# Performance work log

Hardware: AMD Instinct MI355X
Metric: run time of the kernel (lower is better)

Reference implementation:

```python
import jax, jax.numpy as jnp
import numpy as np

B, N, C = 16, 64, 512


def _ln(x, g, b, eps=1e-5):
    m = x.mean(-1, keepdims=True)
    v = ((x - m) ** 2).mean(-1, keepdims=True)
    return (x - m) * jax.lax.rsqrt(v + eps) * g + b


def _layer(x, edge, WA, WB, WE, WU, WV, ge, be, gv, bv):
    # x: (B, N, C); edge: (B, N, N, C) with edge[b, i, j] for pair (end=i, start=j)
    n = x.shape[1]
    res = x
    Vix = x @ WA.T  # end-node (i) features
    Vjx = x @ WB.T  # start-node (j) features
    e_lin = edge @ WE.T
    # 'ev,bvc->bec' with end/start one-hots == broadcast gather over i / j
    m = Vix[:, :, None, :] + Vjx[:, None, :, :] + e_lin
    edge = edge + jax.nn.relu(_ln(m, ge, be))
    e = jax.nn.softmax(jax.nn.sigmoid(edge), axis=2)  # softmax over start-node axis j
    Ujx = x @ WV.T  # gathered at start node j
    # end.T scatter == sum over j of e[b,i,j,c] * Ujx[b,j,c]
    agg = jnp.einsum('bijc,bjc->bic', e, Ujx) / n
    x = x @ WU.T + agg
    x = jax.nn.relu(res + _ln(x, gv, bv))
    return x, edge


def setup_inputs() -> dict:
    key = jax.random.key(0)
    ks = jax.random.split(key, 12)
    scale = float(np.sqrt(2.0 / C))
    inp = {
        "x": jax.random.normal(ks[0], (B, N, C), jnp.float32),
        "edge": jax.random.normal(ks[1], (B, N * N, C), jnp.float32),
    }
    names = ["WA1", "WB1", "WE1", "WU1", "WV1", "WA2", "WB2", "WE2", "WU2", "WV2"]
    for i, nm in enumerate(names):
        inp[nm] = jax.random.normal(ks[2 + i], (C, C), jnp.float32) * scale
    for nm in ["ge1", "gv1", "ge2", "gv2"]:
        inp[nm] = jnp.ones((C,), jnp.float32)
    for nm in ["be1", "bv1", "be2", "bv2"]:
        inp[nm] = jnp.zeros((C,), jnp.float32)
    return inp


def reference(x, edge, WA1, WB1, WE1, WU1, WV1, WA2, WB2, WE2, WU2, WV2,
              ge1, be1, gv1, bv1, ge2, be2, gv2, bv2):
    b, _, c = edge.shape
    n = x.shape[1]
    edge = edge.reshape(b, n, n, c)
    x, edge = _layer(x, edge, WA1, WB1, WE1, WU1, WV1, ge1, be1, gv1, bv1)
    x, edge = _layer(x, edge, WA2, WB2, WE2, WU2, WV2, ge2, be2, gv2, bv2)
    return x, edge.reshape(b, n * n, c)
```

## Files before the change

kernel.cpp:

```cpp
#include <hip/hip_runtime.h>
#include <math.h>

#define CD 512
#define NNODE 64
#define TPAD 520

typedef __attribute__((ext_vector_type(8)))  short bfrag8;
typedef __attribute__((ext_vector_type(8)))  short sv8;
typedef __attribute__((ext_vector_type(4)))  short sv4;
typedef __attribute__((ext_vector_type(16))) float f32x16;

__device__ __forceinline__ unsigned short f2bf(float f) {
    union { float f; unsigned u; } v; v.f = f;
    unsigned r = (v.u + 0x7fffu + ((v.u >> 16) & 1u)) >> 16;
    return (unsigned short)r;
}
__device__ __forceinline__ float bf2f(unsigned short u) {
    union { unsigned u; float f; } v; v.u = ((unsigned)u) << 16;
    return v.f;
}

__global__ void pack32_k(const float* __restrict__ W0, const float* __restrict__ W1,
                         const float* __restrict__ W2, const float* __restrict__ W3,
                         const float* __restrict__ W4, const float* __restrict__ W5,
                         const float* __restrict__ W6, const float* __restrict__ W7,
                         const float* __restrict__ W8, const float* __restrict__ W9,
                         unsigned short* __restrict__ out)
{
    const float* Ws[10] = {W0,W1,W2,W3,W4,W5,W6,W7,W8,W9};
    int kt = blockIdx.x, ct = blockIdx.y, wi = blockIdx.z, l = threadIdx.x;
    const float* W = Ws[wi];
    int c  = ct * 32 + (l & 31);
    int k0 = kt * 16 + (l >> 5) * 8;
    const float* src = W + (size_t)c * CD + k0;
    unsigned short o[8];
    #pragma unroll
    for (int i = 0; i < 8; ++i) o[i] = f2bf(src[i]);
    unsigned short* dst = out + (size_t)wi * 262144 + ((size_t)(kt * 16 + ct) * 64 + l) * 8;
    *(bfrag8*)dst = *(bfrag8*)o;
}

__global__ __launch_bounds__(512, 4) void proj_mfma(
    const float* __restrict__ A, const unsigned short* __restrict__ Bp4,
    float* __restrict__ O0, float* __restrict__ O1,
    float* __restrict__ O2, float* __restrict__ O3)
{
    __shared__ unsigned short tile[64 * TPAD];
    const int rb = blockIdx.x * 64, widx = blockIdx.y;
    float* outs[4] = {O0,O1,O2,O3};
    float* out = outs[widx];
    const unsigned short* Bp = Bp4 + (size_t)widx * 262144;
    const int t = threadIdx.x, l = t & 63, w = t >> 6;
    const int stripe = w & 1, H = w >> 1;

    const float* src = A + (size_t)rb * CD;
    #pragma unroll 4
    for (int it = 0; it < 16; ++it) {
        int flat = it * 2048 + t * 4;
        float4 v4 = *(const float4*)(src + flat);
        int r = flat >> 9, c = flat & 511;
        sv4 pk; pk.x = (short)f2bf(v4.x); pk.y = (short)f2bf(v4.y);
        pk.z = (short)f2bf(v4.z); pk.w = (short)f2bf(v4.w);
        *(sv4*)(tile + r * TPAD + c) = pk;
    }
    __syncthreads();

    f32x16 acc[4] = {};
    const unsigned short* aptr = tile + (size_t)(stripe * 32 + (l & 31)) * TPAD + (l >> 5) * 8;
    const unsigned short* bptr = Bp + ((size_t)(H * 4) * 64 + l) * 8;

    bfrag8 a0, a1, b0[4], b1[4];
    a0 = *(const bfrag8*)aptr;
    #pragma unroll
    for (int tt = 0; tt < 4; ++tt) b0[tt] = *(const bfrag8*)(bptr + tt * 512);
    for (int k2 = 0; k2 < 16; ++k2) {
        int kt1 = 2 * k2 + 1;
        a1 = *(const bfrag8*)(aptr + kt1 * 16);
        #pragma unroll
        for (int tt = 0; tt < 4; ++tt) b1[tt] = *(const bfrag8*)(bptr + (size_t)kt1 * 8192 + tt * 512);
        #pragma unroll
        for (int tt = 0; tt < 4; ++tt)
            acc[tt] = __builtin_amdgcn_mfma_f32_32x32x16_bf16(a0, b0[tt], acc[tt], 0, 0, 0);
        int kt2 = (k2 == 15) ? 31 : (2 * k2 + 2);
        a0 = *(const bfrag8*)(aptr + kt2 * 16);
        #pragma unroll
        for (int tt = 0; tt < 4; ++tt) b0[tt] = *(const bfrag8*)(bptr + (size_t)kt2 * 8192 + tt * 512);
        #pragma unroll
        for (int tt = 0; tt < 4; ++tt)
            acc[tt] = __builtin_amdgcn_mfma_f32_32x32x16_bf16(a1, b1[tt], acc[tt], 0, 0, 0);
    }
    const int cbase = H * 128 + (l & 31);
    #pragma unroll
    for (int r = 0; r < 16; ++r) {
        int rl = (r & 3) + 8 * (r >> 2) + 4 * (l >> 5);
        int row = rb + stripe * 32 + rl;
        #pragma unroll
        for (int tt = 0; tt < 4; ++tt)
            out[(size_t)row * CD + cbase + tt * 32] = acc[tt][r];
    }
}

template<bool INBF, bool OUTBF>
__global__ __launch_bounds__(512, 4) void edge_mfma(
    const void* __restrict__ einv, void* __restrict__ eoutv,
    const float* __restrict__ Vix, const float* __restrict__ Vjx,
    const float* __restrict__ Ujx, const unsigned short* __restrict__ Bp,
    const float* __restrict__ ge, const float* __restrict__ be,
    float* __restrict__ agg)
{
    __shared__ unsigned short tile[64 * TPAD];
    __shared__ float sums[64][4][2];

    const int bi = blockIdx.x;
    const int brow = bi & ~63;
    const int t = threadIdx.x, l = t & 63, w = t >> 6;
    const int stripe = w & 1, H = w >> 1;

    if (INBF) {
        const unsigned short* src = (const unsigned short*)einv + (size_t)bi * 65536;
        #pragma unroll 4
        for (int it = 0; it < 8; ++it) {
            int flat = it * 4096 + t * 8;
            int r = flat >> 9, c = flat & 511;
            *(sv8*)(tile + r * TPAD + c) = *(const sv8*)(src + flat);
        }
    } else {
        const float* src = (const float*)einv + (size_t)bi * 32768;
        #pragma unroll 4
        for (int it = 0; it < 16; ++it) {
            int flat = it * 2048 + t * 4;
            float4 v4 = *(const float4*)(src + flat);
            int r = flat >> 9, c = flat & 511;
            sv4 pk; pk.x = (short)f2bf(v4.x); pk.y = (short)f2bf(v4.y);
            pk.z = (short)f2bf(v4.z); pk.w = (short)f2bf(v4.w);
            *(sv4*)(tile + r * TPAD + c) = pk;
        }
    }
    __syncthreads();

    f32x16 acc[4] = {};
    const unsigned short* aptr = tile + (size_t)(stripe * 32 + (l & 31)) * TPAD + (l >> 5) * 8;
    const unsigned short* bptr = Bp + ((size_t)(H * 4) * 64 + l) * 8;

    bfrag8 a0, a1, b0[4], b1[4];
    a0 = *(const bfrag8*)aptr;
    #pragma unroll
    for (int tt = 0; tt < 4; ++tt) b0[tt] = *(const bfrag8*)(bptr + tt * 512);
    for (int k2 = 0; k2 < 16; ++k2) {
        int kt1 = 2 * k2 + 1;
        a1 = *(const bfrag8*)(aptr + kt1 * 16);
        #pragma unroll
        for (int tt = 0; tt < 4; ++tt) b1[tt] = *(const bfrag8*)(bptr + (size_t)kt1 * 8192 + tt * 512);
        #pragma unroll
        for (int tt = 0; tt < 4; ++tt)
            acc[tt] = __builtin_amdgcn_mfma_f32_32x32x16_bf16(a0, b0[tt], acc[tt], 0, 0, 0);
        int kt2 = (k2 == 15) ? 31 : (2 * k2 + 2);
        a0 = *(const bfrag8*)(aptr + kt2 * 16);
        #pragma unroll
        for (int tt = 0; tt < 4; ++tt) b0[tt] = *(const bfrag8*)(bptr + (size_t)kt2 * 8192 + tt * 512);
        #pragma unroll
        for (int tt = 0; tt < 4; ++tt)
            acc[tt] = __builtin_amdgcn_mfma_f32_32x32x16_bf16(a1, b1[tt], acc[tt], 0, 0, 0);
    }

    const int cbase = H * 128 + (l & 31);
    float vix[4], gev[4], bev[4];
    #pragma unroll
    for (int tt = 0; tt < 4; ++tt) {
        int c = cbase + tt * 32;
        vix[tt] = Vix[(size_t)bi * CD + c];
        gev[tt] = ge[c]; bev[tt] = be[c];
    }
    float s1[16], s2[16];
    #pragma unroll
    for (int r = 0; r < 16; ++r) {
        int rl = (r & 3) + 8 * (r >> 2) + 4 * (l >> 5);
        int rt = stripe * 32 + rl;
        const float* vjr = Vjx + (size_t)(brow + rt) * CD;
        float a1_ = 0.f, a2_ = 0.f;
        #pragma unroll
        for (int tt = 0; tt < 4; ++tt) {
            float m = acc[tt][r] + vix[tt] + vjr[cbase + tt * 32];
            acc[tt][r] = m;
            a1_ += m; a2_ = fmaf(m, m, a2_);
        }
        s1[r] = a1_; s2[r] = a2_;
    }
    #pragma unroll
    for (int off = 1; off < 32; off <<= 1) {
        #pragma unroll
        for (int r = 0; r < 16; ++r) {
            s1[r] += __shfl_xor(s1[r], off, 64);
            s2[r] += __shfl_xor(s2[r], off, 64);
        }
    }
    if ((l & 31) == 0) {
        #pragma unroll
        for (int r = 0; r < 16; ++r) {
            int rl = (r & 3) + 8 * (r >> 2) + 4 * (l >> 5);
            int rt = stripe * 32 + rl;
            sums[rt][H][0] = s1[r]; sums[rt][H][1] = s2[r];
        }
    }
    __syncthreads();

    #pragma unroll
    for (int r = 0; r < 16; ++r) {
        int rl = (r & 3) + 8 * (r >> 2) + 4 * (l >> 5);
        int rt = stripe * 32 + rl;
        float t1 = sums[rt][0][0] + sums[rt][1][0] + sums[rt][2][0] + sums[rt][3][0];
        float t2 = sums[rt][0][1] + sums[rt][1][1] + sums[rt][2][1] + sums[rt][3][1];
        float mean = t1 * (1.f / 512.f);
        float var  = t2 * (1.f / 512.f) - mean * mean;
        float rs   = rsqrtf(var + 1e-5f);
        unsigned short* trow = tile + (size_t)rt * TPAD;
        #pragma unroll
        for (int tt = 0; tt < 4; ++tt) {
            int c = cbase + tt * 32;
            float ln  = (acc[tt][r] - mean) * rs * gev[tt] + bev[tt];
            float env = bf2f(trow[c]) + fmaxf(ln, 0.f);
            if (OUTBF) ((unsigned short*)eoutv)[(size_t)bi * 65536 + rt * 512 + c] = f2bf(env);
            else       ((float*)eoutv)[(size_t)bi * 32768 + rt * 512 + c] = env;
            float sg = 1.f / (1.f + __expf(-env));
            trow[c] = f2bf(__expf(sg));
        }
    }
    __syncthreads();

    {
        int c = t;
        const float* uj = Ujx + (size_t)brow * CD + c;
        float den = 0.f, num = 0.f;
        #pragma unroll 8
        for (int j = 0; j < NNODE; ++j) {
            float wv = bf2f(tile[j * TPAD + c]);
            float uv = uj[(size_t)j * CD];
            den += wv; num = fmaf(wv, uv, num);
        }
        agg[(size_t)bi * CD + c] = num / (den * (float)NNODE);
    }
}

__global__ __launch_bounds__(256) void xupd_kernel(
    const float* __restrict__ res,
    const float* __restrict__ XU,
    const float* __restrict__ aggp,
    const float* __restrict__ gv, const float* __restrict__ bv,
    float* __restrict__ xout)
{
    int r = blockIdx.x * 4 + (threadIdx.x >> 6);
    int lane = threadIdx.x & 63;
    const float* xu = XU + (size_t)r * CD;
    const float* ag = aggp + (size_t)r * CD;
    float y[8]; float s1 = 0.f, s2 = 0.f;
    #pragma unroll
    for (int u = 0; u < 8; ++u) {
        int c = lane + u * 64;
        float v = xu[c] + ag[c];
        y[u] = v; s1 += v; s2 += v * v;
    }
    #pragma unroll
    for (int off = 32; off > 0; off >>= 1) {
        s1 += __shfl_xor(s1, off, 64);
        s2 += __shfl_xor(s2, off, 64);
    }
    float mean = s1 * (1.f / 512.f);
    float var  = s2 * (1.f / 512.f) - mean * mean;
    float rs   = rsqrtf(var + 1e-5f);
    const float* rr = res + (size_t)r * CD;
    float* xo = xout + (size_t)r * CD;
    #pragma unroll
    for (int u = 0; u < 8; ++u) {
        int c = lane + u * 64;
        float ln = (y[u] - mean) * rs * gv[c] + bv[c];
        xo[c] = fmaxf(rr[c] + ln, 0.f);
    }
}

extern "C" void kernel_launch(void* const* d_in, const int* in_sizes, int n_in,
                              void* d_out, int out_size, void* d_ws, size_t ws_size,
                              hipStream_t stream)
{
    const float* x    = (const float*)d_in[0];
    const float* edge = (const float*)d_in[1];
    const float* W[10];
    for (int i = 0; i < 10; ++i) W[i] = (const float*)d_in[2 + i];
    const float* ge1 = (const float*)d_in[12];
    const float* gv1 = (const float*)d_in[13];
    const float* ge2 = (const float*)d_in[14];
    const float* gv2 = (const float*)d_in[15];
    const float* be1 = (const float*)d_in[16];
    const float* bv1 = (const float*)d_in[17];
    const float* be2 = (const float*)d_in[18];
    const float* bv2 = (const float*)d_in[19];

    char* wsb = (char*)d_ws;
    unsigned short* P32 = (unsigned short*)wsb;
    float* Vix = (float*)(wsb + (size_t)6  * 1048576);
    float* Vjx = (float*)(wsb + (size_t)8  * 1048576);
    float* Ujx = (float*)(wsb + (size_t)10 * 1048576);
    float* XU  = (float*)(wsb + (size_t)12 * 1048576);
    float* agg = (float*)(wsb + (size_t)14 * 1048576);
    float* x1  = (float*)(wsb + (size_t)16 * 1048576);

    float* xout  = (float*)d_out;
    float* eintF = xout + (size_t)524288;

    pack32_k<<<dim3(32, 16, 10), 64, 0, stream>>>(
        W[0], W[1], W[4], W[3], W[5], W[6], W[9], W[8], W[2], W[7], P32);

#define PW(i) (P32 + (size_t)(i) * 262144)
    proj_mfma<<<dim3(16, 4), 512, 0, stream>>>(x, PW(0), Vix, Vjx, Ujx, XU);
    edge_mfma<false, true><<<1024, 512, 0, stream>>>(edge, eintF, Vix, Vjx, Ujx,
                                                     PW(8), ge1, be1, agg);
    xupd_kernel<<<256, 256, 0, stream>>>(x, XU, agg, gv1, bv1, x1);
    proj_mfma<<<dim3(16, 4), 512, 0, stream>>>(x1, PW(4), Vix, Vjx, Ujx, XU);
    edge_mfma<true, false><<<1024, 512, 0, stream>>>(eintF, eintF, Vix, Vjx, Ujx,
                                                     PW(9), ge2, be2, agg);
    xupd_kernel<<<256, 256, 0, stream>>>(x1, XU, agg, gv2, bv2, xout);
#undef PW
}
```

Measured before the change: 492.0 us.

## Retile edge MFMA per-wave to 64x64, async LDS loads, register-resident softmax aggregation

Changes the edge GEMM wave tiling from a 32x128 stripe per wave to a 64-row by 64-column tile per wave using a 2x2 set of MFMA accumulators, and prefetches the first B fragments before the tile load. The bf16 input path now uses global_load_lds to copy straight into LDS without going through registers. LayerNorm row statistics are reduced once per row into a shared rowstat array instead of every lane summing the partials. The softmax weights stay in registers and the aggregation over j is done per lane with a cross-half shuffle, which removes the tile write-back and re-read. The cost is more loads of Vjx and Ujx per thread and a different register-pressure profile.

```diff
diff --git a/kernel.cpp b/kernel.cpp
--- a/kernel.cpp
+++ b/kernel.cpp
@@ -18,6 +18,12 @@
 __device__ __forceinline__ float bf2f(unsigned short u) {
     union { unsigned u; float f; } v; v.u = ((unsigned)u) << 16;
     return v.f;
+}
+
+__device__ __forceinline__ void gload_lds16(const void* g, void* s) {
+    __builtin_amdgcn_global_load_lds(
+        (const __attribute__((address_space(1))) unsigned int*)g,
+        (__attribute__((address_space(3))) unsigned int*)s, 16, 0, 0);
 }
 
 __global__ void pack32_k(const float* __restrict__ W0, const float* __restrict__ W1,
@@ -109,20 +115,25 @@
     float* __restrict__ agg)
 {
     __shared__ unsigned short tile[64 * TPAD];
-    __shared__ float sums[64][4][2];
+    __shared__ float sums[64][8][2];
+    __shared__ float rowstat[64][2];
 
     const int bi = blockIdx.x;
     const int brow = bi & ~63;
     const int t = threadIdx.x, l = t & 63, w = t >> 6;
-    const int stripe = w & 1, H = w >> 1;
+    const int hi = l >> 5;
+
+    const unsigned short* bptr = Bp + ((size_t)(2 * w) * 64 + l) * 8;
+    bfrag8 b0[2], b1[2];
+    #pragma unroll
+    for (int ct = 0; ct < 2; ++ct) b0[ct] = *(const bfrag8*)(bptr + ct * 512);
 
     if (INBF) {
         const unsigned short* src = (const unsigned short*)einv + (size_t)bi * 65536;
-        #pragma unroll 4
+        #pragma unroll
         for (int it = 0; it < 8; ++it) {
-            int flat = it * 4096 + t * 8;
-            int r = flat >> 9, c = flat & 511;
-            *(sv8*)(tile + r * TPAD + c) = *(const sv8*)(src + flat);
+            int row = it * 8 + w;
+            gload_lds16(src + (size_t)row * 512 + l * 8, tile + (size_t)row * TPAD);
         }
     } else {
         const float* src = (const float*)einv + (size_t)bi * 32768;
@@ -138,106 +149,125 @@
     }
     __syncthreads();
 
-    f32x16 acc[4] = {};
-    const unsigned short* aptr = tile + (size_t)(stripe * 32 + (l & 31)) * TPAD + (l >> 5) * 8;
-    const unsigned short* bptr = Bp + ((size_t)(H * 4) * 64 + l) * 8;
-
-    bfrag8 a0, a1, b0[4], b1[4];
-    a0 = *(const bfrag8*)aptr;
-    #pragma unroll
-    for (int tt = 0; tt < 4; ++tt) b0[tt] = *(const bfrag8*)(bptr + tt * 512);
+    f32x16 acc[2][2] = {};
+    const unsigned short* aptr = tile + (size_t)(l & 31) * TPAD + hi * 8;
+
+    bfrag8 a0[2], a1[2];
+    #pragma unroll
+    for (int rt = 0; rt < 2; ++rt) a0[rt] = *(const bfrag8*)(aptr + rt * 32 * TPAD);
     for (int k2 = 0; k2 < 16; ++k2) {
         int kt1 = 2 * k2 + 1;
-        a1 = *(const bfrag8*)(aptr + kt1 * 16);
-        #pragma unroll
-        for (int tt = 0; tt < 4; ++tt) b1[tt] = *(const bfrag8*)(bptr + (size_t)kt1 * 8192 + tt * 512);
-        #pragma unroll
-        for (int tt = 0; tt < 4; ++tt)
-            acc[tt] = __builtin_amdgcn_mfma_f32_32x32x16_bf16(a0, b0[tt], acc[tt], 0, 0, 0);
+        #pragma unroll
+        for (int rt = 0; rt < 2; ++rt) a1[rt] = *(const bfrag8*)(aptr + rt * 32 * TPAD + kt1 * 16);
+        #pragma unroll
+        for (int ct = 0; ct < 2; ++ct) b1[ct] = *(const bfrag8*)(bptr + (size_t)kt1 * 8192 + ct * 512);
+        #pragma unroll
+        for (int rt = 0; rt < 2; ++rt)
+            #pragma unroll
+            for (int ct = 0; ct < 2; ++ct)
+                acc[rt][ct] = __builtin_amdgcn_mfma_f32_32x32x16_bf16(a0[rt], b0[ct], acc[rt][ct], 0, 0, 0);
         int kt2 = (k2 == 15) ? 31 : (2 * k2 + 2);
-        a0 = *(const bfrag8*)(aptr + kt2 * 16);
-        #pragma unroll
-        for (int tt = 0; tt < 4; ++tt) b0[tt] = *(const bfrag8*)(bptr + (size_t)kt2 * 8192 + tt * 512);
-        #pragma unroll
-        for (int tt = 0; tt < 4; ++tt)
-            acc[tt] = __builtin_amdgcn_mfma_f32_32x32x16_bf16(a1, b1[tt], acc[tt], 0, 0, 0);
-    }
-
-    const int cbase = H * 128 + (l & 31);
-    float vix[4], gev[4], bev[4];
-    #pragma unroll
-    for (int tt = 0; tt < 4; ++tt) {
-        int c = cbase + tt * 32;
-        vix[tt] = Vix[(size_t)bi * CD + c];
-        gev[tt] = ge[c]; bev[tt] = be[c];
-    }
-    float s1[16], s2[16];
-    #pragma unroll
-    for (int r = 0; r < 16; ++r) {
-        int rl = (r & 3) + 8 * (r >> 2) + 4 * (l >> 5);
-        int rt = stripe * 32 + rl;
-        const float* vjr = Vjx + (size_t)(brow + rt) * CD;
-        float a1_ = 0.f, a2_ = 0.f;
-        #pragma unroll
-        for (int tt = 0; tt < 4; ++tt) {
-            float m = acc[tt][r] + vix[tt] + vjr[cbase + tt * 32];
-            acc[tt][r] = m;
-            a1_ += m; a2_ = fmaf(m, m, a2_);
-        }
-        s1[r] = a1_; s2[r] = a2_;
-    }
-    #pragma unroll
-    for (int off = 1; off < 32; off <<= 1) {
+        #pragma unroll
+        for (int rt = 0; rt < 2; ++rt) a0[rt] = *(const bfrag8*)(aptr + rt * 32 * TPAD + kt2 * 16);
+        #pragma unroll
+        for (int ct = 0; ct < 2; ++ct) b0[ct] = *(const bfrag8*)(bptr + (size_t)kt2 * 8192 + ct * 512);
+        #pragma unroll
+        for (int rt = 0; rt < 2; ++rt)
+            #pragma unroll
+            for (int ct = 0; ct < 2; ++ct)
+                acc[rt][ct] = __builtin_amdgcn_mfma_f32_32x32x16_bf16(a1[rt], b1[ct], acc[rt][ct], 0, 0, 0);
+    }
+
+    const int c0 = w * 64 + (l & 31);
+    const float* VixB = Vix + (size_t)bi * CD;
+    const float vix0 = VixB[c0], vix1 = VixB[c0 + 32];
+    const float gev[2] = {ge[c0], ge[c0 + 32]};
+    const float bev[2] = {be[c0], be[c0 + 32]};
+    const float* VjxB = Vjx + (size_t)brow * CD;
+
+    #pragma unroll
+    for (int rt = 0; rt < 2; ++rt) {
+        float s1[16], s2[16];
         #pragma unroll
         for (int r = 0; r < 16; ++r) {
-            s1[r] += __shfl_xor(s1[r], off, 64);
-            s2[r] += __shfl_xor(s2[r], off, 64);
-        }
-    }
-    if ((l & 31) == 0) {
-        #pragma unroll
-        for (int r = 0; r < 16; ++r) {
-            int rl = (r & 3) + 8 * (r >> 2) + 4 * (l >> 5);
-            int rt = stripe * 32 + rl;
-            sums[rt][H][0] = s1[r]; sums[rt][H][1] = s2[r];
+            int rl = (r & 3) + 8 * (r >> 2) + 4 * hi;
+            int row = rt * 32 + rl;
+            const float* vjr = VjxB + (size_t)row * CD;
+            float m0 = acc[rt][0][r] + vix0 + vjr[c0];
+            float m1 = acc[rt][1][r] + vix1 + vjr[c0 + 32];
+            acc[rt][0][r] = m0; acc[rt][1][r] = m1;
+            s1[r] = m0 + m1; s2[r] = m0 * m0 + m1 * m1;
+        }
+        #pragma unroll
+        for (int off = 1; off < 32; off <<= 1) {
+            #pragma unroll
+            for (int r = 0; r < 16; ++r) {
+                s1[r] += __shfl_xor(s1[r], off, 64);
+                s2[r] += __shfl_xor(s2[r], off, 64);
+            }
+        }
+        if ((l & 31) == 0) {
+            #pragma unroll
+            for (int r = 0; r < 16; ++r) {
+                int rl = (r & 3) + 8 * (r >> 2) + 4 * hi;
+                float2 p; p.x = s1[r]; p.y = s2[r];
+                *(float2*)&sums[rt * 32 + rl][w][0] = p;
+            }
         }
     }
     __syncthreads();
 
-    #pragma unroll
-    for (int r = 0; r < 16; ++r) {
-        int rl = (r & 3) + 8 * (r >> 2) + 4 * (l >> 5);
-        int rt = stripe * 32 + rl;
-        float t1 = sums[rt][0][0] + sums[rt][1][0] + sums[rt][2][0] + sums[rt][3][0];
-        float t2 = sums[rt][0][1] + sums[rt][1][1] + sums[rt][2][1] + sums[rt][3][1];
+    if (t < 64) {
+        float t1 = 0.f, t2 = 0.f;
+        #pragma unroll
+        for (int ww = 0; ww < 8; ++ww) { t1 += sums[t][ww][0]; t2 += sums[t][ww][1]; }
         float mean = t1 * (1.f / 512.f);
         float var  = t2 * (1.f / 512.f) - mean * mean;
-        float rs   = rsqrtf(var + 1e-5f);
-        unsigned short* trow = tile + (size_t)rt * TPAD;
-        #pragma unroll
-        for (int tt = 0; tt < 4; ++tt) {
-            int c = cbase + tt * 32;
-            float ln  = (acc[tt][r] - mean) * rs * gev[tt] + bev[tt];
-            float env = bf2f(trow[c]) + fmaxf(ln, 0.f);
-            if (OUTBF) ((unsigned short*)eoutv)[(size_t)bi * 65536 + rt * 512 + c] = f2bf(env);
-            else       ((float*)eoutv)[(size_t)bi * 32768 + rt * 512 + c] = env;
-            float sg = 1.f / (1.f + __expf(-env));
-            trow[c] = f2bf(__expf(sg));
-        }
+        float2 mr; mr.x = mean; mr.y = rsqrtf(var + 1e-5f);
+        *(float2*)&rowstat[t][0] = mr;
     }
     __syncthreads();
 
-    {
-        int c = t;
-        const float* uj = Ujx + (size_t)brow * CD + c;
+    #pragma unroll
+    for (int rt = 0; rt < 2; ++rt) {
+        #pragma unroll
+        for (int r = 0; r < 16; ++r) {
+            int rl = (r & 3) + 8 * (r >> 2) + 4 * hi;
+            int row = rt * 32 + rl;
+            float2 mr = *(const float2*)&rowstat[row][0];
+            const unsigned short* trow = tile + (size_t)row * TPAD;
+            #pragma unroll
+            for (int ct = 0; ct < 2; ++ct) {
+                int c = c0 + ct * 32;
+                float ln  = (acc[rt][ct][r] - mr.x) * mr.y * gev[ct] + bev[ct];
+                float env = bf2f(trow[c]) + fmaxf(ln, 0.f);
+                if (OUTBF) ((unsigned short*)eoutv)[(size_t)bi * 65536 + row * 512 + c] = f2bf(env);
+                else       ((float*)eoutv)[(size_t)bi * 32768 + row * 512 + c] = env;
+                float sg = 1.f / (1.f + __expf(-env));
+                acc[rt][ct][r] = __expf(sg);
+            }
+        }
+    }
+
+    const float* UjxB = Ujx + (size_t)brow * CD;
+    #pragma unroll
+    for (int ct = 0; ct < 2; ++ct) {
+        int c = c0 + ct * 32;
         float den = 0.f, num = 0.f;
-        #pragma unroll 8
-        for (int j = 0; j < NNODE; ++j) {
-            float wv = bf2f(tile[j * TPAD + c]);
-            float uv = uj[(size_t)j * CD];
-            den += wv; num = fmaf(wv, uv, num);
-        }
-        agg[(size_t)bi * CD + c] = num / (den * (float)NNODE);
+        #pragma unroll
+        for (int rt = 0; rt < 2; ++rt) {
+            #pragma unroll
+            for (int r = 0; r < 16; ++r) {
+                int rl = (r & 3) + 8 * (r >> 2) + 4 * hi;
+                int row = rt * 32 + rl;
+                float wv = acc[rt][ct][r];
+                float uv = UjxB[(size_t)row * CD + c];
+                den += wv; num = fmaf(wv, uv, num);
+            }
+        }
+        den += __shfl_xor(den, 32, 64);
+        num += __shfl_xor(num, 32, 64);
+        if (l < 32) agg[(size_t)bi * CD + c] = num / (den * (float)NNODE);
     }
 }
 
```

Result: slower. 545.8 us (+10.9%).

## Fuse node-update LayerNorm into edge kernel and halve projection row tile

Applied to the files above, without the earlier changes.

The separate xupd kernel is removed. Each edge_mfma block (one end node per block) now computes its aggregate, adds XU, does a block-wide LayerNorm reduction through shared memory and writes the updated node features directly. This drops two launches and the agg round trip through global memory. The projection kernel also moves from 64-row to 32-row tiles, so it launches twice as many blocks with two column tiles per wave, trading more weight-fragment reloads for more parallelism.

```diff
diff --git a/kernel.cpp b/kernel.cpp
--- a/kernel.cpp
+++ b/kernel.cpp
@@ -45,17 +45,16 @@
     float* __restrict__ O0, float* __restrict__ O1,
     float* __restrict__ O2, float* __restrict__ O3)
 {
-    __shared__ unsigned short tile[64 * TPAD];
-    const int rb = blockIdx.x * 64, widx = blockIdx.y;
+    __shared__ unsigned short tile[32 * TPAD];
+    const int rb = blockIdx.x * 32, widx = blockIdx.y;
     float* outs[4] = {O0,O1,O2,O3};
     float* out = outs[widx];
     const unsigned short* Bp = Bp4 + (size_t)widx * 262144;
     const int t = threadIdx.x, l = t & 63, w = t >> 6;
-    const int stripe = w & 1, H = w >> 1;
 
     const float* src = A + (size_t)rb * CD;
     #pragma unroll 4
-    for (int it = 0; it < 16; ++it) {
+    for (int it = 0; it < 8; ++it) {
         int flat = it * 2048 + t * 4;
         float4 v4 = *(const float4*)(src + flat);
         int r = flat >> 9, c = flat & 511;
@@ -65,38 +64,38 @@
     }
     __syncthreads();
 
-    f32x16 acc[4] = {};
-    const unsigned short* aptr = tile + (size_t)(stripe * 32 + (l & 31)) * TPAD + (l >> 5) * 8;
-    const unsigned short* bptr = Bp + ((size_t)(H * 4) * 64 + l) * 8;
-
-    bfrag8 a0, a1, b0[4], b1[4];
+    f32x16 acc[2] = {};
+    const unsigned short* aptr = tile + (size_t)(l & 31) * TPAD + (l >> 5) * 8;
+    const unsigned short* bptr = Bp + ((size_t)(2 * w) * 64 + l) * 8;
+
+    bfrag8 a0, a1, b0[2], b1[2];
     a0 = *(const bfrag8*)aptr;
     #pragma unroll
-    for (int tt = 0; tt < 4; ++tt) b0[tt] = *(const bfrag8*)(bptr + tt * 512);
+    for (int ct = 0; ct < 2; ++ct) b0[ct] = *(const bfrag8*)(bptr + ct * 512);
     for (int k2 = 0; k2 < 16; ++k2) {
         int kt1 = 2 * k2 + 1;
         a1 = *(const bfrag8*)(aptr + kt1 * 16);
         #pragma unroll
-        for (int tt = 0; tt < 4; ++tt) b1[tt] = *(const bfrag8*)(bptr + (size_t)kt1 * 8192 + tt * 512);
-        #pragma unroll
-        for (int tt = 0; tt < 4; ++tt)
-            acc[tt] = __builtin_amdgcn_mfma_f32_32x32x16_bf16(a0, b0[tt], acc[tt], 0, 0, 0);
+        for (int ct = 0; ct < 2; ++ct) b1[ct] = *(const bfrag8*)(bptr + (size_t)kt1 * 8192 + ct * 512);
+        #pragma unroll
+        for (int ct = 0; ct < 2; ++ct)
+            acc[ct] = __builtin_amdgcn_mfma_f32_32x32x16_bf16(a0, b0[ct], acc[ct], 0, 0, 0);
         int kt2 = (k2 == 15) ? 31 : (2 * k2 + 2);
         a0 = *(const bfrag8*)(aptr + kt2 * 16);
         #pragma unroll
-        for (int tt = 0; tt < 4; ++tt) b0[tt] = *(const bfrag8*)(bptr + (size_t)kt2 * 8192 + tt * 512);
-        #pragma unroll
-        for (int tt = 0; tt < 4; ++tt)
-            acc[tt] = __builtin_amdgcn_mfma_f32_32x32x16_bf16(a1, b1[tt], acc[tt], 0, 0, 0);
-    }
-    const int cbase = H * 128 + (l & 31);
+        for (int ct = 0; ct < 2; ++ct) b0[ct] = *(const bfrag8*)(bptr + (size_t)kt2 * 8192 + ct * 512);
+        #pragma unroll
+        for (int ct = 0; ct < 2; ++ct)
+            acc[ct] = __builtin_amdgcn_mfma_f32_32x32x16_bf16(a1, b1[ct], acc[ct], 0, 0, 0);
+    }
+    const int cbase = w * 64 + (l & 31);
     #pragma unroll
     for (int r = 0; r < 16; ++r) {
         int rl = (r & 3) + 8 * (r >> 2) + 4 * (l >> 5);
-        int row = rb + stripe * 32 + rl;
-        #pragma unroll
-        for (int tt = 0; tt < 4; ++tt)
-            out[(size_t)row * CD + cbase + tt * 32] = acc[tt][r];
+        int row = rb + rl;
+        #pragma unroll
+        for (int ct = 0; ct < 2; ++ct)
+            out[(size_t)row * CD + cbase + ct * 32] = acc[ct][r];
     }
 }
 
@@ -106,10 +105,13 @@
     const float* __restrict__ Vix, const float* __restrict__ Vjx,
     const float* __restrict__ Ujx, const unsigned short* __restrict__ Bp,
     const float* __restrict__ ge, const float* __restrict__ be,
-    float* __restrict__ agg)
+    const float* __restrict__ XU, const float* __restrict__ xres,
+    const float* __restrict__ gv, const float* __restrict__ bv,
+    float* __restrict__ xout)
 {
     __shared__ unsigned short tile[64 * TPAD];
     __shared__ float sums[64][4][2];
+    __shared__ float xs1[8], xs2[8];
 
     const int bi = blockIdx.x;
     const int brow = bi & ~63;
@@ -237,43 +239,25 @@
             float uv = uj[(size_t)j * CD];
             den += wv; num = fmaf(wv, uv, num);
         }
-        agg[(size_t)bi * CD + c] = num / (den * (float)NNODE);
-    }
-}
-
-__global__ __launch_bounds__(256) void xupd_kernel(
-    const float* __restrict__ res,
-    const float* __restrict__ XU,
-    const float* __restrict__ aggp,
-    const float* __restrict__ gv, const float* __restrict__ bv,
-    float* __restrict__ xout)
-{
-    int r = blockIdx.x * 4 + (threadIdx.x >> 6);
-    int lane = threadIdx.x & 63;
-    const float* xu = XU + (size_t)r * CD;
-    const float* ag = aggp + (size_t)r * CD;
-    float y[8]; float s1 = 0.f, s2 = 0.f;
-    #pragma unroll
-    for (int u = 0; u < 8; ++u) {
-        int c = lane + u * 64;
-        float v = xu[c] + ag[c];
-        y[u] = v; s1 += v; s2 += v * v;
-    }
-    #pragma unroll
-    for (int off = 32; off > 0; off >>= 1) {
-        s1 += __shfl_xor(s1, off, 64);
-        s2 += __shfl_xor(s2, off, 64);
-    }
-    float mean = s1 * (1.f / 512.f);
-    float var  = s2 * (1.f / 512.f) - mean * mean;
-    float rs   = rsqrtf(var + 1e-5f);
-    const float* rr = res + (size_t)r * CD;
-    float* xo = xout + (size_t)r * CD;
-    #pragma unroll
-    for (int u = 0; u < 8; ++u) {
-        int c = lane + u * 64;
-        float ln = (y[u] - mean) * rs * gv[c] + bv[c];
-        xo[c] = fmaxf(rr[c] + ln, 0.f);
+        float aggv = num / (den * (float)NNODE);
+
+        float v = XU[(size_t)bi * CD + c] + aggv;
+        float s1x = v, s2x = v * v;
+        #pragma unroll
+        for (int off = 1; off < 64; off <<= 1) {
+            s1x += __shfl_xor(s1x, off, 64);
+            s2x += __shfl_xor(s2x, off, 64);
+        }
+        if (l == 0) { xs1[w] = s1x; xs2[w] = s2x; }
+        __syncthreads();
+        float t1 = 0.f, t2 = 0.f;
+        #pragma unroll
+        for (int ww = 0; ww < 8; ++ww) { t1 += xs1[ww]; t2 += xs2[ww]; }
+        float mean = t1 * (1.f / 512.f);
+        float var  = t2 * (1.f / 512.f) - mean * mean;
+        float rs   = rsqrtf(var + 1e-5f);
+        float ln   = (v - mean) * rs * gv[c] + bv[c];
+        xout[(size_t)bi * CD + c] = fmaxf(xres[(size_t)bi * CD + c] + ln, 0.f);
     }
 }
 
@@ -300,7 +284,6 @@
     float* Vjx = (float*)(wsb + (size_t)8  * 1048576);
     float* Ujx = (float*)(wsb + (size_t)10 * 1048576);
     float* XU  = (float*)(wsb + (size_t)12 * 1048576);
-    float* agg = (float*)(wsb + (size_t)14 * 1048576);
     float* x1  = (float*)(wsb + (size_t)16 * 1048576);
 
     float* xout  = (float*)d_out;
@@ -310,13 +293,11 @@
         W[0], W[1], W[4], W[3], W[5], W[6], W[9], W[8], W[2], W[7], P32);
 
 #define PW(i) (P32 + (size_t)(i) * 262144)
-    proj_mfma<<<dim3(16, 4), 512, 0, stream>>>(x, PW(0), Vix, Vjx, Ujx, XU);
+    proj_mfma<<<dim3(32, 4), 512, 0, stream>>>(x, PW(0), Vix, Vjx, Ujx, XU);
     edge_mfma<false, true><<<1024, 512, 0, stream>>>(edge, eintF, Vix, Vjx, Ujx,
-                                                     PW(8), ge1, be1, agg);
-    xupd_kernel<<<256, 256, 0, stream>>>(x, XU, agg, gv1, bv1, x1);
-    proj_mfma<<<dim3(16, 4), 512, 0, stream>>>(x1, PW(4), Vix, Vjx, Ujx, XU);
+                                                     PW(8), ge1, be1, XU, x, gv1, bv1, x1);
+    proj_mfma<<<dim3(32, 4), 512, 0, stream>>>(x1, PW(4), Vix, Vjx, Ujx, XU);
     edge_mfma<true, false><<<1024, 512, 0, stream>>>(eintF, eintF, Vix, Vjx, Ujx,
-                                                     PW(9), ge2, be2, agg);
-    xupd_kernel<<<256, 256, 0, stream>>>(x1, XU, agg, gv2, bv2, xout);
+                                                     PW(9), ge2, be2, XU, x1, gv2, bv2, xout);
 #undef PW
 }
```

After: 496.5 us. No clear change (+0.9%).

## Fuse node update into second projection, aggregate from registers, halve projection row tile

Applied to the files above, without the earlier changes.

Folds the first layer's x-update LayerNorm/residual/ReLU into the prologue of the second projection kernel. Each of the four weight blocks recomputes it redundantly, and block 0 writes x1. This removes one kernel launch and a round trip through memory. The edge kernel now builds the softmax numerator and denominator in registers during the epilogue, reduced through shuffles and a small shared buffer. This replaces writing exp values back into the shared tile and rereading them in a per-column loop. Projection blocks now cover 32 rows instead of 64, doubling the grid, and a second XU buffer avoids overwriting the one still in use.

```diff
diff --git a/kernel.cpp b/kernel.cpp
--- a/kernel.cpp
+++ b/kernel.cpp
@@ -40,63 +40,112 @@
     *(bfrag8*)dst = *(bfrag8*)o;
 }
 
+template<bool FUSE>
 __global__ __launch_bounds__(512, 4) void proj_mfma(
     const float* __restrict__ A, const unsigned short* __restrict__ Bp4,
     float* __restrict__ O0, float* __restrict__ O1,
-    float* __restrict__ O2, float* __restrict__ O3)
-{
-    __shared__ unsigned short tile[64 * TPAD];
-    const int rb = blockIdx.x * 64, widx = blockIdx.y;
+    float* __restrict__ O2, float* __restrict__ O3,
+    const float* __restrict__ aggp, const float* __restrict__ xres,
+    const float* __restrict__ gvp, const float* __restrict__ bvp,
+    float* __restrict__ x1out)
+{
+    __shared__ unsigned short tile[32 * TPAD];
+    const int rb = blockIdx.x * 32, widx = blockIdx.y;
     float* outs[4] = {O0,O1,O2,O3};
     float* out = outs[widx];
     const unsigned short* Bp = Bp4 + (size_t)widx * 262144;
     const int t = threadIdx.x, l = t & 63, w = t >> 6;
-    const int stripe = w & 1, H = w >> 1;
-
-    const float* src = A + (size_t)rb * CD;
-    #pragma unroll 4
-    for (int it = 0; it < 16; ++it) {
-        int flat = it * 2048 + t * 4;
-        float4 v4 = *(const float4*)(src + flat);
-        int r = flat >> 9, c = flat & 511;
-        sv4 pk; pk.x = (short)f2bf(v4.x); pk.y = (short)f2bf(v4.y);
-        pk.z = (short)f2bf(v4.z); pk.w = (short)f2bf(v4.w);
-        *(sv4*)(tile + r * TPAD + c) = pk;
+
+    if (FUSE) {
+        const int r32 = t >> 4, sub = t & 15, cb = sub * 32;
+        const size_t rowo = (size_t)(rb + r32) * CD + cb;
+        const float* xu = A + rowo;
+        const float* ag = aggp + rowo;
+        float v[32]; float s1 = 0.f, s2 = 0.f;
+        #pragma unroll
+        for (int q = 0; q < 8; ++q) {
+            float4 a4 = *(const float4*)(xu + q * 4);
+            float4 g4 = *(const float4*)(ag + q * 4);
+            float v0 = a4.x + g4.x, v1 = a4.y + g4.y;
+            float v2 = a4.z + g4.z, v3 = a4.w + g4.w;
+            v[q*4+0] = v0; v[q*4+1] = v1; v[q*4+2] = v2; v[q*4+3] = v3;
+            s1 += v0 + v1 + v2 + v3;
+            s2 += v0*v0 + v1*v1 + v2*v2 + v3*v3;
+        }
+        #pragma unroll
+        for (int off = 1; off < 16; off <<= 1) {
+            s1 += __shfl_xor(s1, off, 64);
+            s2 += __shfl_xor(s2, off, 64);
+        }
+        float mean = s1 * (1.f / 512.f);
+        float var  = s2 * (1.f / 512.f) - mean * mean;
+        float rs   = rsqrtf(var + 1e-5f);
+        const float* rr = xres + rowo;
+        unsigned short* trow = tile + r32 * TPAD + cb;
+        float* xo = x1out + rowo;
+        #pragma unroll
+        for (int q = 0; q < 8; ++q) {
+            float4 r4 = *(const float4*)(rr + q * 4);
+            float4 g4 = *(const float4*)(gvp + cb + q * 4);
+            float4 b4 = *(const float4*)(bvp + cb + q * 4);
+            float x0 = fmaxf(r4.x + (v[q*4+0]-mean)*rs*g4.x + b4.x, 0.f);
+            float x1_ = fmaxf(r4.y + (v[q*4+1]-mean)*rs*g4.y + b4.y, 0.f);
+            float x2 = fmaxf(r4.z + (v[q*4+2]-mean)*rs*g4.z + b4.z, 0.f);
+            float x3 = fmaxf(r4.w + (v[q*4+3]-mean)*rs*g4.w + b4.w, 0.f);
+            sv4 pk; pk.x = (short)f2bf(x0); pk.y = (short)f2bf(x1_);
+            pk.z = (short)f2bf(x2); pk.w = (short)f2bf(x3);
+            *(sv4*)(trow + q * 4) = pk;
+            if (widx == 0) {
+                float4 o4; o4.x = x0; o4.y = x1_; o4.z = x2; o4.w = x3;
+                *(float4*)(xo + q * 4) = o4;
+            }
+        }
+    } else {
+        const float* src = A + (size_t)rb * CD;
+        #pragma unroll 4
+        for (int it = 0; it < 8; ++it) {
+            int flat = it * 2048 + t * 4;
+            float4 v4 = *(const float4*)(src + flat);
+            int r = flat >> 9, c = flat & 511;
+            sv4 pk; pk.x = (short)f2bf(v4.x); pk.y = (short)f2bf(v4.y);
+            pk.z = (short)f2bf(v4.z); pk.w = (short)f2bf(v4.w);
+            *(sv4*)(tile + r * TPAD + c) = pk;
+        }
     }
     __syncthreads();
 
-    f32x16 acc[4] = {};
-    const unsigned short* aptr = tile + (size_t)(stripe * 32 + (l & 31)) * TPAD + (l >> 5) * 8;
-    const unsigned short* bptr = Bp + ((size_t)(H * 4) * 64 + l) * 8;
-
-    bfrag8 a0, a1, b0[4], b1[4];
+    f32x16 acc[2] = {};
+    const unsigned short* aptr = tile + (size_t)(l & 31) * TPAD + (l >> 5) * 8;
+    const unsigned short* bptr = Bp + ((size_t)(2 * w) * 64 + l) * 8;
+
+    bfrag8 a0, a1, b0[2], b1[2];
     a0 = *(const bfrag8*)aptr;
     #pragma unroll
-    for (int tt = 0; tt < 4; ++tt) b0[tt] = *(const bfrag8*)(bptr + tt * 512);
+    for (int ct = 0; ct < 2; ++ct) b0[ct] = *(const bfrag8*)(bptr + ct * 512);
     for (int k2 = 0; k2 < 16; ++k2) {
         int kt1 = 2 * k2 + 1;
         a1 = *(const bfrag8*)(aptr + kt1 * 16);
         #pragma unroll
-        for (int tt = 0; tt < 4; ++tt) b1[tt] = *(const bfrag8*)(bptr + (size_t)kt1 * 8192 + tt * 512);
-        #pragma unroll
-        for (int tt = 0; tt < 4; ++tt)
-            acc[tt] = __builtin_amdgcn_mfma_f32_32x32x16_bf16(a0, b0[tt], acc[tt], 0, 0, 0);
+        for (int ct = 0; ct < 2; ++ct) b1[ct] = *(const bfrag8*)(bptr + (size_t)kt1 * 8192 + ct * 512);
+        #pragma unroll
+        for (int ct = 0; ct < 2; ++ct)
+            acc[ct] = __builtin_amdgcn_mfma_f32_32x32x16_bf16(a0, b0[ct], acc[ct], 0, 0, 0);
         int kt2 = (k2 == 15) ? 31 : (2 * k2 + 2);
         a0 = *(const bfrag8*)(aptr + kt2 * 16);
         #pragma unroll
-        for (int tt = 0; tt < 4; ++tt) b0[tt] = *(const bfrag8*)(bptr + (size_t)kt2 * 8192 + tt * 512);
-        #pragma unroll
-        for (int tt = 0; tt < 4; ++tt)
-            acc[tt] = __builtin_amdgcn_mfma_f32_32x32x16_bf16(a1, b1[tt], acc[tt], 0, 0, 0);
-    }
-    const int cbase = H * 128 + (l & 31);
+        for (int ct = 0; ct < 2; ++ct) b0[ct] = *(const bfrag8*)(bptr + (size_t)kt2 * 8192 + ct * 512);
+        #pragma unroll
+        for (int ct = 0; ct < 2; ++ct)
+            acc[ct] = __builtin_amdgcn_mfma_f32_32x32x16_bf16(a1, b1[ct], acc[ct], 0, 0, 0);
+    }
+    const int cbase = w * 64 + (l & 31);
     #pragma unroll
     for (int r = 0; r < 16; ++r) {
         int rl = (r & 3) + 8 * (r >> 2) + 4 * (l >> 5);
-        int row = rb + stripe * 32 + rl;
-        #pragma unroll
-        for (int tt = 0; tt < 4; ++tt)
-            out[(size_t)row * CD + cbase + tt * 32] = acc[tt][r];
+        int row = rb + rl;
+        #pragma unroll
+        for (int ct = 0; ct < 2; ++ct)
+            out[(size_t)row * CD + cbase + ct * 32] = acc[ct][r];
     }
 }
 
@@ -110,6 +159,7 @@
 {
     __shared__ unsigned short tile[64 * TPAD];
     __shared__ float sums[64][4][2];
+    __shared__ float red[4][4][2][2][32];
 
     const int bi = blockIdx.x;
     const int brow = bi & ~63;
@@ -204,6 +254,8 @@
     }
     __syncthreads();
 
+    const float* UjxB = Ujx + (size_t)brow * CD;
+    float den[4] = {0.f,0.f,0.f,0.f}, num[4] = {0.f,0.f,0.f,0.f};
     #pragma unroll
     for (int r = 0; r < 16; ++r) {
         int rl = (r & 3) + 8 * (r >> 2) + 4 * (l >> 5);
@@ -213,7 +265,8 @@
         float mean = t1 * (1.f / 512.f);
         float var  = t2 * (1.f / 512.f) - mean * mean;
         float rs   = rsqrtf(var + 1e-5f);
-        unsigned short* trow = tile + (size_t)rt * TPAD;
+        const unsigned short* trow = tile + (size_t)rt * TPAD;
+        const float* ujr = UjxB + (size_t)rt * CD;
         #pragma unroll
         for (int tt = 0; tt < 4; ++tt) {
             int c = cbase + tt * 32;
@@ -222,22 +275,32 @@
             if (OUTBF) ((unsigned short*)eoutv)[(size_t)bi * 65536 + rt * 512 + c] = f2bf(env);
             else       ((float*)eoutv)[(size_t)bi * 32768 + rt * 512 + c] = env;
             float sg = 1.f / (1.f + __expf(-env));
-            trow[c] = f2bf(__expf(sg));
+            float wv = bf2f(f2bf(__expf(sg)));
+            den[tt] += wv;
+            num[tt] = fmaf(wv, ujr[c], num[tt]);
+        }
+    }
+    #pragma unroll
+    for (int tt = 0; tt < 4; ++tt) {
+        den[tt] += __shfl_xor(den[tt], 32, 64);
+        num[tt] += __shfl_xor(num[tt], 32, 64);
+    }
+    if (l < 32) {
+        #pragma unroll
+        for (int tt = 0; tt < 4; ++tt) {
+            red[tt][H][stripe][0][l] = den[tt];
+            red[tt][H][stripe][1][l] = num[tt];
         }
     }
     __syncthreads();
 
-    {
-        int c = t;
-        const float* uj = Ujx + (size_t)brow * CD + c;
-        float den = 0.f, num = 0.f;
-        #pragma unroll 8
-        for (int j = 0; j < NNODE; ++j) {
-            float wv = bf2f(tile[j * TPAD + c]);
-            float uv = uj[(size_t)j * CD];
-            den += wv; num = fmaf(wv, uv, num);
-        }
-        agg[(size_t)bi * CD + c] = num / (den * (float)NNODE);
+    if (stripe == 0 && l < 32) {
+        #pragma unroll
+        for (int tt = 0; tt < 4; ++tt) {
+            float d  = red[tt][H][0][0][l] + red[tt][H][1][0][l];
+            float nm = red[tt][H][0][1][l] + red[tt][H][1][1][l];
+            agg[(size_t)bi * CD + H * 128 + l + tt * 32] = nm / (d * (float)NNODE);
+        }
     }
 }
 
@@ -299,9 +362,10 @@
     float* Vix = (float*)(wsb + (size_t)6  * 1048576);
     float* Vjx = (float*)(wsb + (size_t)8  * 1048576);
     float* Ujx = (float*)(wsb + (size_t)10 * 1048576);
-    float* XU  = (float*)(wsb + (size_t)12 * 1048576);
+    float* XUa = (float*)(wsb + (size_t)12 * 1048576);
     float* agg = (float*)(wsb + (size_t)14 * 1048576);
     float* x1  = (float*)(wsb + (size_t)16 * 1048576);
+    float* XUb = (float*)(wsb + (size_t)18 * 1048576);
 
     float* xout  = (float*)d_out;
     float* eintF = xout + (size_t)524288;
@@ -310,13 +374,14 @@
         W[0], W[1], W[4], W[3], W[5], W[6], W[9], W[8], W[2], W[7], P32);
 
 #define PW(i) (P32 + (size_t)(i) * 262144)
-    proj_mfma<<<dim3(16, 4), 512, 0, stream>>>(x, PW(0), Vix, Vjx, Ujx, XU);
+    proj_mfma<false><<<dim3(32, 4), 512, 0, stream>>>(x, PW(0), Vix, Vjx, Ujx, XUa,
+                                                      nullptr, nullptr, nullptr, nullptr, nullptr);
     edge_mfma<false, true><<<1024, 512, 0, stream>>>(edge, eintF, Vix, Vjx, Ujx,
                                                      PW(8), ge1, be1, agg);
-    xupd_kernel<<<256, 256, 0, stream>>>(x, XU, agg, gv1, bv1, x1);
-    proj_mfma<<<dim3(16, 4), 512, 0, stream>>>(x1, PW(4), Vix, Vjx, Ujx, XU);
+    proj_mfma<true><<<dim3(32, 4), 512, 0, stream>>>(XUa, PW(4), Vix, Vjx, Ujx, XUb,
+                                                     agg, x, gv1, bv1, x1);
     edge_mfma<true, false><<<1024, 512, 0, stream>>>(eintF, eintF, Vix, Vjx, Ujx,
                                                      PW(9), ge2, be2, agg);
-    xupd_kernel<<<256, 256, 0, stream>>>(x1, XU, agg, gv2, bv2, xout);
+    xupd_kernel<<<256, 256, 0, stream>>>(x1, XUb, agg, gv2, bv2, xout);
 #undef PW
 }
```

Measured after the change: 512.9 us. 4.2% more time.
